# Kernel optimization log

Measured on AMD Instinct MI355X. Metric: run time of the kernel, lower is better.

## Reference

```python
import jax, jax.numpy as jnp
import numpy as np
import math

B, C, F, H, W, K = 2, 4, 512, 8, 1024, 3
DH = F // H

def _rotary(x):
    # lucidrains-style rotary: interleaved pairs, x:[..., seq, d]
    d, seq = x.shape[-1], x.shape[-2]
    inv = 1.0 / (10000.0 ** (jnp.arange(0, d, 2, dtype=jnp.float32) / d))
    freqs = jnp.arange(seq, dtype=jnp.float32)[:, None] * inv[None, :]  # [seq, d/2]
    freqs = jnp.repeat(freqs, 2, axis=-1)                               # [seq, d]
    cos, sin = jnp.cos(freqs), jnp.sin(freqs)
    xp = x.reshape(x.shape[:-1] + (d // 2, 2))
    rot = jnp.stack([-xp[..., 1], xp[..., 0]], axis=-1).reshape(x.shape)
    return x * cos + rot * sin

def _mc_linear(x, w):
    # per-channel position-wise linear: x [b,c,f,w], w [c, f_out, f_in]
    return jnp.einsum('bcfw,cgf->bcgw', x, w)

def _conv(x, w, bias):
    # Conv2d(C, C, (1,K), padding=(0,(K-1)//2)); w [O=c, I=c, 1, K]
    pad = (K - 1) // 2
    y = jax.lax.conv_general_dilated(x, w, (1, 1), [(0, 0), (pad, pad)],
                                     dimension_numbers=('NCHW', 'OIHW', 'NCHW'))
    return y + bias[None, :, None, None]

def _heads(x):
    # [b,c,f,w] -> [b,c,H,w,dh]
    b, c, f, w = x.shape
    return x.transpose(0, 1, 3, 2).reshape(b, c, w, H, DH).transpose(0, 1, 3, 2, 4)

def setup_inputs() -> dict:
    key = jax.random.key(0)
    ks = jax.random.split(key, 12)
    p = lambda k, shp: jax.random.normal(k, shp, dtype=jnp.float32) * 0.02
    return {
        'x': jax.random.normal(ks[0], (B, C, F, W), dtype=jnp.float32),
        'prev_qk': jax.random.normal(ks[1], (B, C, H, W, W), dtype=jnp.float32),
        'mask': jax.random.normal(ks[2], (1, 1, 1, W, W), dtype=jnp.float32),
        'wq_lin': p(ks[3], (C, F, F)), 'wq_conv': p(ks[4], (C, C, 1, K)), 'bq_conv': jnp.zeros((C,), jnp.float32),
        'wk_lin': p(ks[5], (C, F, F)), 'wk_conv': p(ks[6], (C, C, 1, K)), 'bk_conv': jnp.zeros((C,), jnp.float32),
        'wv_lin': p(ks[7], (C, F, F)), 'wv_conv': p(ks[8], (C, C, 1, K)), 'bv_conv': jnp.zeros((C,), jnp.float32),
        'wo_lin': p(ks[9], (C, F, F)),
    }

def reference(x, prev_qk, mask, wq_lin, wq_conv, bq_conv, wk_lin, wk_conv, bk_conv,
              wv_lin, wv_conv, bv_conv, wo_lin):
    b, c, f, w = x.shape
    q = _rotary(_heads(_conv(_mc_linear(x, wq_lin), wq_conv, bq_conv)))   # [b,c,H,w,dh]
    k = _rotary(_heads(_conv(_mc_linear(x, wk_lin), wk_conv, bk_conv)))
    v = _heads(_conv(_mc_linear(x, wv_lin), wv_conv, bv_conv))
    qk = jnp.einsum('bchqd,bchkd->bchqk', q, k) / math.sqrt(f) + prev_qk + mask
    a = jnp.einsum('bchqk,bchkd->bchqd', jax.nn.softmax(qk, axis=-1), v)  # [b,c,H,w,dh]
    a = a.transpose(0, 1, 3, 2, 4).reshape(b, c, w, f).transpose(0, 1, 3, 2)  # [b,c,f,w]
    out = _mc_linear(a, wo_lin)
    return out, qk
```

## Files before the change

### kernel.cpp

```cpp
#include <hip/hip_runtime.h>
#include <hip/hip_bf16.h>
#include <math.h>

typedef unsigned short u16;
typedef unsigned int   u32;
typedef __attribute__((ext_vector_type(8))) short short8;
typedef __attribute__((ext_vector_type(4))) float f32x4;

#define Bn 2
#define Cn 4
#define Fn 512
#define Hn 8
#define Wn 1024
#define DHn 64
#define FW (Fn*Wn)
#define BCFW (Bn*Cn*Fn*Wn)

__device__ __forceinline__ u16 f2bf(float f) {
  u32 u = __builtin_bit_cast(u32, f);
  u += 0x7fffu + ((u >> 16) & 1u);
  return (u16)(u >> 16);
}
__device__ __forceinline__ float bf2f(u16 h) {
  u32 u = ((u32)h) << 16;
  return __builtin_bit_cast(float, u);
}
__device__ __forceinline__ u32 pack2(u16 a, u16 b) { return (u32)a | ((u32)b << 16); }

__global__ __launch_bounds__(256) void wconv_kernel(
    const float* __restrict__ wq, const float* __restrict__ wk,
    const float* __restrict__ wv, const float* __restrict__ wo,
    u16* __restrict__ wb3, u16* __restrict__ wob) {
  int g = blockIdx.x * 256 + threadIdx.x;
  int t = g >> 18;
  int off = (g & 0x3FFFF) * 4;
  const float* src = (t == 0) ? wq : (t == 1) ? wk : (t == 2) ? wv : wo;
  float4 v = *(const float4*)(src + off);
  u16* dst = (t < 3) ? (wb3 + (size_t)t * 1048576 + off) : (wob + off);
  uint2 p;
  p.x = pack2(f2bf(v.x), f2bf(v.y));
  p.y = pack2(f2bf(v.z), f2bf(v.w));
  *(uint2*)dst = p;
}

__global__ __launch_bounds__(256) void xT_kernel(const float* __restrict__ x, u16* __restrict__ xT) {
  __shared__ __align__(16) u16 T[64 * 72];
  int w0 = blockIdx.x * 64, f0 = blockIdx.y * 64, bc = blockIdx.z;
  int tid = threadIdx.x;
  int r = tid >> 2, g = tid & 3;
  const float* src = x + ((size_t)(bc * Fn + f0 + r)) * Wn + w0 + g * 16;
#pragma unroll
  for (int u = 0; u < 4; u++) {
    float4 v = *(const float4*)(src + u * 4);
    int cb = g * 16 + u * 4;
    T[r * 72 + cb + 0] = f2bf(v.x);
    T[r * 72 + cb + 1] = f2bf(v.y);
    T[r * 72 + cb + 2] = f2bf(v.z);
    T[r * 72 + cb + 3] = f2bf(v.w);
  }
  __syncthreads();
  int wl = tid >> 2, fg = tid & 3;
  u16 ov[16];
#pragma unroll
  for (int u = 0; u < 16; u++) ov[u] = T[(fg * 16 + u) * 72 + wl];
  u16* dst = xT + ((size_t)(bc * Wn + w0 + wl)) * Fn + f0 + fg * 16;
  uint4 o0, o1;
  o0.x = pack2(ov[0], ov[1]);  o0.y = pack2(ov[2], ov[3]);
  o0.z = pack2(ov[4], ov[5]);  o0.w = pack2(ov[6], ov[7]);
  o1.x = pack2(ov[8], ov[9]);  o1.y = pack2(ov[10], ov[11]);
  o1.z = pack2(ov[12], ov[13]); o1.w = pack2(ov[14], ov[15]);
  *(uint4*)(dst) = o0;
  *(uint4*)(dst + 8) = o1;
}

__global__ __launch_bounds__(256) void gemm_bt_kernel(
    const u16* __restrict__ Abase, const u16* __restrict__ BTbase,
    u16* __restrict__ Cb, float* __restrict__ Cf) {
  __shared__ __align__(16) u16 As[128 * 40];
  __shared__ __align__(16) u16 Bs[128 * 40];
  int tile = blockIdx.x;
  int bc = blockIdx.y;
  int p = blockIdx.z;
  int m0 = (tile & 3) * 128, n0 = (tile >> 2) * 128;
  const u16* A = Abase + ((size_t)(p * 4 + (bc & 3))) * (512 * 512) + (size_t)m0 * 512;
  const u16* BT = BTbase + (size_t)bc * (1024 * 512) + (size_t)n0 * 512;
  int tid = threadIdx.x, wave = tid >> 6, lane = tid & 63;
  int quad = lane >> 4, l16 = lane & 15;
  int wm = (wave >> 1) * 64, wn = (wave & 1) * 64;
  f32x4 acc[4][4];
#pragma unroll
  for (int i = 0; i < 4; i++)
#pragma unroll
    for (int j = 0; j < 4; j++) acc[i][j] = (f32x4){0.f, 0.f, 0.f, 0.f};
  for (int k0 = 0; k0 < 512; k0 += 32) {
    __syncthreads();
    {
      int c0 = tid, c1 = tid + 256;
      int r = c0 >> 2, o = c0 & 3;
      *(uint4*)&As[r * 40 + o * 8] = *(const uint4*)(A + (size_t)r * 512 + k0 + o * 8);
      *(uint4*)&Bs[r * 40 + o * 8] = *(const uint4*)(BT + (size_t)r * 512 + k0 + o * 8);
      r = c1 >> 2; o = c1 & 3;
      *(uint4*)&As[r * 40 + o * 8] = *(const uint4*)(A + (size_t)r * 512 + k0 + o * 8);
      *(uint4*)&Bs[r * 40 + o * 8] = *(const uint4*)(BT + (size_t)r * 512 + k0 + o * 8);
    }
    __syncthreads();
    short8 af[4], bfr[4];
#pragma unroll
    for (int i = 0; i < 4; i++) af[i] = *(const short8*)&As[(wm + i * 16 + l16) * 40 + quad * 8];
#pragma unroll
    for (int j = 0; j < 4; j++) bfr[j] = *(const short8*)&Bs[(wn + j * 16 + l16) * 40 + quad * 8];
#pragma unroll
    for (int i = 0; i < 4; i++)
#pragma unroll
      for (int j = 0; j < 4; j++)
        acc[i][j] = __builtin_amdgcn_mfma_f32_16x16x32_bf16(af[i], bfr[j], acc[i][j], 0, 0, 0);
  }
  size_t coff = (size_t)(Cb ? (p * 8 + bc) : bc) * FW;
#pragma unroll
  for (int i = 0; i < 4; i++)
#pragma unroll
    for (int j = 0; j < 4; j++)
#pragma unroll
      for (int reg = 0; reg < 4; reg++) {
        int row = m0 + wm + i * 16 + quad * 4 + reg;
        int col = n0 + wn + j * 16 + l16;
        if (Cb) Cb[coff + (size_t)row * 1024 + col] = f2bf(acc[i][j][reg]);
        else    Cf[coff + (size_t)row * 1024 + col] = acc[i][j][reg];
      }
}

__global__ __launch_bounds__(256) void conv_kernel(
    const u16* __restrict__ lin3, u16* __restrict__ conv3,
    const float* __restrict__ wqc, const float* __restrict__ wkc, const float* __restrict__ wvc,
    const float* __restrict__ bq, const float* __restrict__ bk, const float* __restrict__ bv) {
  int w = blockIdx.x * 256 + threadIdx.x;
  int f = blockIdx.y;
  int b = blockIdx.z;
  const float* wcs[3] = {wqc, wkc, wvc};
  const float* bs[3] = {bq, bk, bv};
#pragma unroll
  for (int p = 0; p < 3; p++) {
    const float* wc = wcs[p];
    float acc[4];
#pragma unroll
    for (int o = 0; o < 4; o++) acc[o] = bs[p][o];
#pragma unroll
    for (int i = 0; i < 4; i++) {
      size_t base = ((size_t)((p * 2 + b) * 4 + i) * Fn + f) * Wn + w;
      float xm = (w > 0) ? bf2f(lin3[base - 1]) : 0.f;
      float x0 = bf2f(lin3[base]);
      float xp = (w < Wn - 1) ? bf2f(lin3[base + 1]) : 0.f;
#pragma unroll
      for (int o = 0; o < 4; o++) {
        const float* wr = wc + (o * 4 + i) * 3;
        acc[o] += wr[0] * xm + wr[1] * x0 + wr[2] * xp;
      }
    }
#pragma unroll
    for (int o = 0; o < 4; o++)
      conv3[((size_t)((p * 2 + b) * 4 + o) * Fn + f) * Wn + w] = f2bf(acc[o]);
  }
}

__global__ __launch_bounds__(256) void rot_kernel(
    const u16* __restrict__ conv3, u16* __restrict__ Qb, u16* __restrict__ Kb) {
  __shared__ __align__(16) u16 T[64 * 72];
  int w0 = blockIdx.x * 64;
  int t = blockIdx.y >> 3;
  int h = blockIdx.y & 7;
  int bc = blockIdx.z;
  int b = bc >> 2, c = bc & 3;
  const u16* src = conv3 + ((size_t)((t * 2 + b) * 4 + c) * Fn + h * 64) * Wn;
  int tid = threadIdx.x;
  {
    int dl = tid >> 2, g = tid & 3;
    const u16* s = src + (size_t)dl * Wn + w0 + g * 16;
    *(uint4*)&T[dl * 72 + g * 16] = *(const uint4*)(s);
    *(uint4*)&T[dl * 72 + g * 16 + 8] = *(const uint4*)(s + 8);
  }
  __syncthreads();
  int wl = tid >> 2, dg = tid & 3;
  int pos = w0 + wl;
  u16 ov[16];
#pragma unroll
  for (int u = 0; u < 16; u += 2) {
    int d = dg * 16 + u;
    float x0 = bf2f(T[d * 72 + wl]);
    float x1 = bf2f(T[(d + 1) * 72 + wl]);
    float inv = exp2f(-(float)d * (13.287712379549449f / 64.f));
    float th = (float)pos * inv;
    float sn, cs;
    sincosf(th, &sn, &cs);
    ov[u] = f2bf(x0 * cs - x1 * sn);
    ov[u + 1] = f2bf(x1 * cs + x0 * sn);
  }
  u16* dst = (t == 0 ? Qb : Kb) + ((size_t)(bc * 8 + h) * Wn + pos) * 64 + dg * 16;
  uint4 o0, o1;
  o0.x = pack2(ov[0], ov[1]);  o0.y = pack2(ov[2], ov[3]);
  o0.z = pack2(ov[4], ov[5]);  o0.w = pack2(ov[6], ov[7]);
  o1.x = pack2(ov[8], ov[9]);  o1.y = pack2(ov[10], ov[11]);
  o1.z = pack2(ov[12], ov[13]); o1.w = pack2(ov[14], ov[15]);
  *(uint4*)(dst) = o0;
  *(uint4*)(dst + 8) = o1;
}

__global__ __launch_bounds__(256) void attn_kernel(
    const u16* __restrict__ Qb, const u16* __restrict__ Kb, const u16* __restrict__ Vt,
    const float* __restrict__ prev, const float* __restrict__ maskp,
    float* __restrict__ qkp, u16* __restrict__ Abuf) {
  __shared__ __align__(16) u16 Ks[128 * 72];
  __shared__ __align__(16) u16 Vs[64 * 136];
  __shared__ __align__(16) u16 Ps[128 * 136];
  const int bch = blockIdx.y;
  const int q0 = blockIdx.x * 128;
  const u16* Qg = Qb + (size_t)bch * 65536;
  const u16* Kg = Kb + (size_t)bch * 65536;
  const u16* Vg = Vt + (size_t)bch * 65536;
  const float* prevb = prev + (size_t)bch * 1048576;
  float* qkb = qkp + (size_t)bch * 1048576;
  int tid = threadIdx.x, wave = tid >> 6, lane = tid & 63;
  int quad = lane >> 4, l16 = lane & 15;
  const float SCALE = 0.044194173824159216f;

  short8 qf[2][2];
#pragma unroll
  for (int rt = 0; rt < 2; rt++)
#pragma unroll
    for (int ks = 0; ks < 2; ks++)
      qf[rt][ks] = *(const short8*)(Qg + (size_t)(q0 + wave * 32 + rt * 16 + l16) * 64 + ks * 32 + quad * 8);

  f32x4 oa[2][4];
  float m_run[2][4], l_run[2][4];
#pragma unroll
  for (int rt = 0; rt < 2; rt++)
#pragma unroll
    for (int j = 0; j < 4; j++) {
      oa[rt][j] = (f32x4){0.f, 0.f, 0.f, 0.f};
      m_run[rt][j] = -INFINITY; l_run[rt][j] = 0.f;
    }

  for (int kt = 0; kt < 8; kt++) {
    int k0 = kt * 128;
    __syncthreads();
#pragma unroll
    for (int t = 0; t < 4; t++) {
      int c = tid + 256 * t;
      { int r = c >> 3, of = c & 7;
        *(uint4*)&Ks[r * 72 + of * 8] = *(const uint4*)(Kg + (size_t)(k0 + r) * 64 + of * 8); }
      { int r = c >> 4, of = c & 15;
        *(uint4*)&Vs[r * 136 + of * 8] = *(const uint4*)(Vg + (size_t)r * Wn + k0 + of * 8); }
    }
    __syncthreads();

    f32x4 s[2][8];
#pragma unroll
    for (int rt = 0; rt < 2; rt++)
#pragma unroll
      for (int ct = 0; ct < 8; ct++) s[rt][ct] = (f32x4){0.f, 0.f, 0.f, 0.f};
#pragma unroll
    for (int ct = 0; ct < 8; ct++) {
#pragma unroll
      for (int ks = 0; ks < 2; ks++) {
        short8 kf = *(const short8*)&Ks[(ct * 16 + l16) * 72 + ks * 32 + quad * 8];
        s[0][ct] = __builtin_amdgcn_mfma_f32_16x16x32_bf16(qf[0][ks], kf, s[0][ct], 0, 0, 0);
        s[1][ct] = __builtin_amdgcn_mfma_f32_16x16x32_bf16(qf[1][ks], kf, s[1][ct], 0, 0, 0);
      }
    }
#pragma unroll
    for (int rt = 0; rt < 2; rt++) {
#pragma unroll
      for (int reg = 0; reg < 4; reg++) {
        int rloc = wave * 32 + rt * 16 + quad * 4 + reg;
        int rg = q0 + rloc;
        const float* pr = prevb + (size_t)rg * Wn + k0 + l16;
        const float* mr = maskp + (size_t)rg * Wn + k0 + l16;
        float* qr = qkb + (size_t)rg * Wn + k0 + l16;
        float tv[8];
#pragma unroll
        for (int ct = 0; ct < 8; ct++) {
          tv[ct] = s[rt][ct][reg] * SCALE + pr[ct * 16] + mr[ct * 16];
          qr[ct * 16] = tv[ct];
        }
        float mx = tv[0];
#pragma unroll
        for (int ct = 1; ct < 8; ct++) mx = fmaxf(mx, tv[ct]);
#pragma unroll
        for (int d = 1; d < 16; d <<= 1) mx = fmaxf(mx, __shfl_xor(mx, d));
        float mn = fmaxf(m_run[rt][reg], mx);
        float alpha = __expf(m_run[rt][reg] - mn);
        m_run[rt][reg] = mn;
        float rs = 0.f;
        int prow = rloc * 136;
#pragma unroll
        for (int ct = 0; ct < 8; ct++) {
          float pv = __expf(tv[ct] - mn);
          rs += pv;
          Ps[prow + ct * 16 + l16] = f2bf(pv);
        }
#pragma unroll
        for (int d = 1; d < 16; d <<= 1) rs += __shfl_xor(rs, d);
        l_run[rt][reg] = l_run[rt][reg] * alpha + rs;
#pragma unroll
        for (int jd = 0; jd < 4; jd++) oa[rt][jd][reg] *= alpha;
      }
    }
    __syncthreads();
#pragma unroll
    for (int ks = 0; ks < 4; ks++) {
      short8 pf0 = *(const short8*)&Ps[(wave * 32 + 0 + l16) * 136 + ks * 32 + quad * 8];
      short8 pf1 = *(const short8*)&Ps[(wave * 32 + 16 + l16) * 136 + ks * 32 + quad * 8];
#pragma unroll
      for (int jd = 0; jd < 4; jd++) {
        short8 vf = *(const short8*)&Vs[(jd * 16 + l16) * 136 + ks * 32 + quad * 8];
        oa[0][jd] = __builtin_amdgcn_mfma_f32_16x16x32_bf16(pf0, vf, oa[0][jd], 0, 0, 0);
        oa[1][jd] = __builtin_amdgcn_mfma_f32_16x16x32_bf16(pf1, vf, oa[1][jd], 0, 0, 0);
      }
    }
  }
  int bc = bch >> 3, h = bch & 7;
#pragma unroll
  for (int rt = 0; rt < 2; rt++)
#pragma unroll
    for (int reg = 0; reg < 4; reg++) {
      int rg = q0 + wave * 32 + rt * 16 + quad * 4 + reg;
      float inv_l = 1.f / l_run[rt][reg];
      u16* dst = Abuf + ((size_t)bc * Wn + rg) * Fn + h * 64 + l16;
#pragma unroll
      for (int jd = 0; jd < 4; jd++)
        dst[jd * 16] = f2bf(oa[rt][jd][reg] * inv_l);
    }
}

extern "C" void kernel_launch(void* const* d_in, const int* in_sizes, int n_in,
                              void* d_out, int out_size, void* d_ws, size_t ws_size,
                              hipStream_t stream) {
  (void)in_sizes; (void)n_in; (void)out_size; (void)ws_size;
  const float* x       = (const float*)d_in[0];
  const float* prev    = (const float*)d_in[1];
  const float* mask    = (const float*)d_in[2];
  const float* wq_lin  = (const float*)d_in[3];
  const float* wq_conv = (const float*)d_in[4];
  const float* bq      = (const float*)d_in[5];
  const float* wk_lin  = (const float*)d_in[6];
  const float* wk_conv = (const float*)d_in[7];
  const float* bk      = (const float*)d_in[8];
  const float* wv_lin  = (const float*)d_in[9];
  const float* wv_conv = (const float*)d_in[10];
  const float* bv      = (const float*)d_in[11];
  const float* wo_lin  = (const float*)d_in[12];

  float* outp = (float*)d_out;
  float* qkp  = outp + (size_t)BCFW;

  char* ws = (char*)d_ws;
  u16* xTb   = (u16*)(ws + 0);
  u16* wb3   = (u16*)(ws + ((size_t)8 << 20));
  u16* wob   = (u16*)(ws + ((size_t)14 << 20));
  u16* lin3  = (u16*)(ws + ((size_t)16 << 20));
  u16* conv3 = (u16*)(ws + ((size_t)40 << 20));
  u16* Qbuf  = lin3;
  u16* Kbuf  = lin3 + (size_t)BCFW;
  u16* Abuf  = lin3 + (size_t)2 * BCFW;
  u16* Vt    = conv3 + (size_t)2 * BCFW;

  wconv_kernel<<<4096, 256, 0, stream>>>(wq_lin, wk_lin, wv_lin, wo_lin, wb3, wob);
  xT_kernel<<<dim3(16, 8, 8), 256, 0, stream>>>(x, xTb);
  gemm_bt_kernel<<<dim3(32, 8, 3), 256, 0, stream>>>(wb3, xTb, lin3, nullptr);
  conv_kernel<<<dim3(4, 512, 2), 256, 0, stream>>>(lin3, conv3, wq_conv, wk_conv, wv_conv, bq, bk, bv);
  rot_kernel<<<dim3(16, 16, 8), 256, 0, stream>>>(conv3, Qbuf, Kbuf);
  attn_kernel<<<dim3(8, 64), 256, 0, stream>>>(Qbuf, Kbuf, Vt, prev, mask, qkp, Abuf);
  gemm_bt_kernel<<<dim3(32, 8, 1), 256, 0, stream>>>(wob, Abuf, nullptr, outp);
}
```

Baseline: 828.8 us.

## Split fused attention into parallel QK/stats kernel and PV kernel

```diff
diff --git a/kernel.cpp b/kernel.cpp
--- a/kernel.cpp
+++ b/kernel.cpp
@@ -204,131 +204,157 @@
   *(uint4*)(dst + 8) = o1;
 }
 
-__global__ __launch_bounds__(256) void attn_kernel(
-    const u16* __restrict__ Qb, const u16* __restrict__ Kb, const u16* __restrict__ Vt,
+__global__ __launch_bounds__(256) void qk_kernel(
+    const u16* __restrict__ Qb, const u16* __restrict__ Kb,
     const float* __restrict__ prev, const float* __restrict__ maskp,
-    float* __restrict__ qkp, u16* __restrict__ Abuf) {
+    float* __restrict__ qkp, float2* __restrict__ stats) {
   __shared__ __align__(16) u16 Ks[128 * 72];
-  __shared__ __align__(16) u16 Vs[64 * 136];
-  __shared__ __align__(16) u16 Ps[128 * 136];
-  const int bch = blockIdx.y;
-  const int q0 = blockIdx.x * 128;
+  __shared__ __align__(16) float Sf[64 * 132];
+  const int q0 = blockIdx.x * 64;
+  const int kt = blockIdx.y;
+  const int k0 = kt * 128;
+  const int bch = blockIdx.z;
   const u16* Qg = Qb + (size_t)bch * 65536;
   const u16* Kg = Kb + (size_t)bch * 65536;
-  const u16* Vg = Vt + (size_t)bch * 65536;
   const float* prevb = prev + (size_t)bch * 1048576;
   float* qkb = qkp + (size_t)bch * 1048576;
   int tid = threadIdx.x, wave = tid >> 6, lane = tid & 63;
   int quad = lane >> 4, l16 = lane & 15;
   const float SCALE = 0.044194173824159216f;
 
-  short8 qf[2][2];
-#pragma unroll
-  for (int rt = 0; rt < 2; rt++)
-#pragma unroll
-    for (int ks = 0; ks < 2; ks++)
-      qf[rt][ks] = *(const short8*)(Qg + (size_t)(q0 + wave * 32 + rt * 16 + l16) * 64 + ks * 32 + quad * 8);
-
-  f32x4 oa[2][4];
-  float m_run[2][4], l_run[2][4];
-#pragma unroll
-  for (int rt = 0; rt < 2; rt++)
-#pragma unroll
-    for (int j = 0; j < 4; j++) {
-      oa[rt][j] = (f32x4){0.f, 0.f, 0.f, 0.f};
-      m_run[rt][j] = -INFINITY; l_run[rt][j] = 0.f;
-    }
+  short8 qf[2];
+#pragma unroll
+  for (int ks = 0; ks < 2; ks++)
+    qf[ks] = *(const short8*)(Qg + (size_t)(q0 + wave * 16 + l16) * 64 + ks * 32 + quad * 8);
+
+#pragma unroll
+  for (int t = 0; t < 4; t++) {
+    int c = tid + 256 * t;
+    int r = c >> 3, o = c & 7;
+    *(uint4*)&Ks[r * 72 + o * 8] = *(const uint4*)(Kg + (size_t)(k0 + r) * 64 + o * 8);
+  }
+  __syncthreads();
+
+  f32x4 acc[8];
+#pragma unroll
+  for (int ct = 0; ct < 8; ct++) acc[ct] = (f32x4){0.f, 0.f, 0.f, 0.f};
+#pragma unroll
+  for (int ct = 0; ct < 8; ct++)
+#pragma unroll
+    for (int ks = 0; ks < 2; ks++) {
+      short8 kf = *(const short8*)&Ks[(ct * 16 + l16) * 72 + ks * 32 + quad * 8];
+      acc[ct] = __builtin_amdgcn_mfma_f32_16x16x32_bf16(qf[ks], kf, acc[ct], 0, 0, 0);
+    }
+
+#pragma unroll
+  for (int ct = 0; ct < 8; ct++)
+#pragma unroll
+    for (int reg = 0; reg < 4; reg++)
+      Sf[(wave * 16 + quad * 4 + reg) * 132 + ct * 16 + l16] = acc[ct][reg] * SCALE;
+  __syncthreads();
+
+  int r = tid >> 2, c0 = (tid & 3) * 32;
+  const float* pr = prevb + (size_t)(q0 + r) * Wn + k0 + c0;
+  const float* mr = maskp + (size_t)(q0 + r) * Wn + k0 + c0;
+  float* qr = qkb + (size_t)(q0 + r) * Wn + k0 + c0;
+  float tv[32];
+  float mx = -INFINITY;
+#pragma unroll
+  for (int u = 0; u < 8; u++) {
+    float4 s4 = *(const float4*)&Sf[r * 132 + c0 + u * 4];
+    float4 p4 = *(const float4*)(pr + u * 4);
+    float4 m4 = *(const float4*)(mr + u * 4);
+    float4 t4;
+    t4.x = s4.x + p4.x + m4.x;  t4.y = s4.y + p4.y + m4.y;
+    t4.z = s4.z + p4.z + m4.z;  t4.w = s4.w + p4.w + m4.w;
+    *(float4*)(qr + u * 4) = t4;
+    tv[u * 4 + 0] = t4.x; tv[u * 4 + 1] = t4.y; tv[u * 4 + 2] = t4.z; tv[u * 4 + 3] = t4.w;
+    mx = fmaxf(mx, fmaxf(fmaxf(t4.x, t4.y), fmaxf(t4.z, t4.w)));
+  }
+  mx = fmaxf(mx, __shfl_xor(mx, 1));
+  mx = fmaxf(mx, __shfl_xor(mx, 2));
+  float sum = 0.f;
+#pragma unroll
+  for (int u = 0; u < 32; u++) sum += __expf(tv[u] - mx);
+  sum += __shfl_xor(sum, 1);
+  sum += __shfl_xor(sum, 2);
+  if ((tid & 3) == 0)
+    stats[((size_t)bch * Wn + q0 + r) * 8 + kt] = make_float2(mx, sum);
+}
+
+__global__ __launch_bounds__(256) void pv_kernel(
+    const float* __restrict__ qkp, const u16* __restrict__ Vt,
+    const float2* __restrict__ stats, u16* __restrict__ Abuf) {
+  __shared__ __align__(16) u16 Ps[64 * 136];
+  __shared__ __align__(16) u16 Vs[64 * 136];
+  __shared__ float Mrow[64], Lrow[64];
+  const int q0 = blockIdx.x * 64;
+  const int bch = blockIdx.y;
+  const float* qkb = qkp + (size_t)bch * 1048576;
+  const u16* Vg = Vt + (size_t)bch * 65536;
+  int tid = threadIdx.x, wave = tid >> 6, lane = tid & 63;
+  int quad = lane >> 4, l16 = lane & 15;
+
+  if (tid < 64) {
+    const float2* st = stats + ((size_t)bch * Wn + q0 + tid) * 8;
+    float M = -INFINITY;
+#pragma unroll
+    for (int kt = 0; kt < 8; kt++) M = fmaxf(M, st[kt].x);
+    float L = 0.f;
+#pragma unroll
+    for (int kt = 0; kt < 8; kt++) L += st[kt].y * __expf(st[kt].x - M);
+    Mrow[tid] = M;
+    Lrow[tid] = 1.f / L;
+  }
+
+  f32x4 oa[4];
+#pragma unroll
+  for (int jd = 0; jd < 4; jd++) oa[jd] = (f32x4){0.f, 0.f, 0.f, 0.f};
+
+  int pr_ = tid >> 2, pc_ = (tid & 3) * 32;
+  float Mr, Li;
 
   for (int kt = 0; kt < 8; kt++) {
     int k0 = kt * 128;
     __syncthreads();
+    if (kt == 0) { Mr = Mrow[pr_]; Li = Lrow[pr_]; }
 #pragma unroll
     for (int t = 0; t < 4; t++) {
       int c = tid + 256 * t;
-      { int r = c >> 3, of = c & 7;
-        *(uint4*)&Ks[r * 72 + of * 8] = *(const uint4*)(Kg + (size_t)(k0 + r) * 64 + of * 8); }
-      { int r = c >> 4, of = c & 15;
-        *(uint4*)&Vs[r * 136 + of * 8] = *(const uint4*)(Vg + (size_t)r * Wn + k0 + of * 8); }
+      int r = c >> 4, o = c & 15;
+      *(uint4*)&Vs[r * 136 + o * 8] = *(const uint4*)(Vg + (size_t)r * Wn + k0 + o * 8);
+    }
+    const float* qr = qkb + (size_t)(q0 + pr_) * Wn + k0 + pc_;
+#pragma unroll
+    for (int u = 0; u < 8; u++) {
+      float4 t4 = *(const float4*)(qr + u * 4);
+      u16 p0 = f2bf(__expf(t4.x - Mr) * Li);
+      u16 p1 = f2bf(__expf(t4.y - Mr) * Li);
+      u16 p2 = f2bf(__expf(t4.z - Mr) * Li);
+      u16 p3 = f2bf(__expf(t4.w - Mr) * Li);
+      uint2 pk; pk.x = pack2(p0, p1); pk.y = pack2(p2, p3);
+      *(uint2*)&Ps[pr_ * 136 + pc_ + u * 4] = pk;
     }
     __syncthreads();
-
-    f32x4 s[2][8];
-#pragma unroll
-    for (int rt = 0; rt < 2; rt++)
-#pragma unroll
-      for (int ct = 0; ct < 8; ct++) s[rt][ct] = (f32x4){0.f, 0.f, 0.f, 0.f};
-#pragma unroll
-    for (int ct = 0; ct < 8; ct++) {
-#pragma unroll
-      for (int ks = 0; ks < 2; ks++) {
-        short8 kf = *(const short8*)&Ks[(ct * 16 + l16) * 72 + ks * 32 + quad * 8];
-        s[0][ct] = __builtin_amdgcn_mfma_f32_16x16x32_bf16(qf[0][ks], kf, s[0][ct], 0, 0, 0);
-        s[1][ct] = __builtin_amdgcn_mfma_f32_16x16x32_bf16(qf[1][ks], kf, s[1][ct], 0, 0, 0);
-      }
-    }
-#pragma unroll
-    for (int rt = 0; rt < 2; rt++) {
-#pragma unroll
-      for (int reg = 0; reg < 4; reg++) {
-        int rloc = wave * 32 + rt * 16 + quad * 4 + reg;
-        int rg = q0 + rloc;
-        const float* pr = prevb + (size_t)rg * Wn + k0 + l16;
-        const float* mr = maskp + (size_t)rg * Wn + k0 + l16;
-        float* qr = qkb + (size_t)rg * Wn + k0 + l16;
-        float tv[8];
-#pragma unroll
-        for (int ct = 0; ct < 8; ct++) {
-          tv[ct] = s[rt][ct][reg] * SCALE + pr[ct * 16] + mr[ct * 16];
-          qr[ct * 16] = tv[ct];
-        }
-        float mx = tv[0];
-#pragma unroll
-        for (int ct = 1; ct < 8; ct++) mx = fmaxf(mx, tv[ct]);
-#pragma unroll
-        for (int d = 1; d < 16; d <<= 1) mx = fmaxf(mx, __shfl_xor(mx, d));
-        float mn = fmaxf(m_run[rt][reg], mx);
-        float alpha = __expf(m_run[rt][reg] - mn);
-        m_run[rt][reg] = mn;
-        float rs = 0.f;
-        int prow = rloc * 136;
-#pragma unroll
-        for (int ct = 0; ct < 8; ct++) {
-          float pv = __expf(tv[ct] - mn);
-          rs += pv;
-          Ps[prow + ct * 16 + l16] = f2bf(pv);
-        }
-#pragma unroll
-        for (int d = 1; d < 16; d <<= 1) rs += __shfl_xor(rs, d);
-        l_run[rt][reg] = l_run[rt][reg] * alpha + rs;
-#pragma unroll
-        for (int jd = 0; jd < 4; jd++) oa[rt][jd][reg] *= alpha;
-      }
-    }
-    __syncthreads();
 #pragma unroll
     for (int ks = 0; ks < 4; ks++) {
-      short8 pf0 = *(const short8*)&Ps[(wave * 32 + 0 + l16) * 136 + ks * 32 + quad * 8];
-      short8 pf1 = *(const short8*)&Ps[(wave * 32 + 16 + l16) * 136 + ks * 32 + quad * 8];
+      short8 pf = *(const short8*)&Ps[(wave * 16 + l16) * 136 + ks * 32 + quad * 8];
 #pragma unroll
       for (int jd = 0; jd < 4; jd++) {
         short8 vf = *(const short8*)&Vs[(jd * 16 + l16) * 136 + ks * 32 + quad * 8];
-        oa[0][jd] = __builtin_amdgcn_mfma_f32_16x16x32_bf16(pf0, vf, oa[0][jd], 0, 0, 0);
-        oa[1][jd] = __builtin_amdgcn_mfma_f32_16x16x32_bf16(pf1, vf, oa[1][jd], 0, 0, 0);
+        oa[jd] = __builtin_amdgcn_mfma_f32_16x16x32_bf16(pf, vf, oa[jd], 0, 0, 0);
       }
     }
   }
   int bc = bch >> 3, h = bch & 7;
 #pragma unroll
-  for (int rt = 0; rt < 2; rt++)
-#pragma unroll
-    for (int reg = 0; reg < 4; reg++) {
-      int rg = q0 + wave * 32 + rt * 16 + quad * 4 + reg;
-      float inv_l = 1.f / l_run[rt][reg];
-      u16* dst = Abuf + ((size_t)bc * Wn + rg) * Fn + h * 64 + l16;
-#pragma unroll
-      for (int jd = 0; jd < 4; jd++)
-        dst[jd * 16] = f2bf(oa[rt][jd][reg] * inv_l);
-    }
+  for (int reg = 0; reg < 4; reg++) {
+    int rg = q0 + wave * 16 + quad * 4 + reg;
+    u16* dst = Abuf + ((size_t)bc * Wn + rg) * Fn + h * 64 + l16;
+#pragma unroll
+    for (int jd = 0; jd < 4; jd++)
+      dst[jd * 16] = f2bf(oa[jd][reg]);
+  }
 }
 
 extern "C" void kernel_launch(void* const* d_in, const int* in_sizes, int n_in,
@@ -362,12 +388,14 @@
   u16* Kbuf  = lin3 + (size_t)BCFW;
   u16* Abuf  = lin3 + (size_t)2 * BCFW;
   u16* Vt    = conv3 + (size_t)2 * BCFW;
+  float2* stats = (float2*)(ws + ((size_t)40 << 20));
 
   wconv_kernel<<<4096, 256, 0, stream>>>(wq_lin, wk_lin, wv_lin, wo_lin, wb3, wob);
   xT_kernel<<<dim3(16, 8, 8), 256, 0, stream>>>(x, xTb);
   gemm_bt_kernel<<<dim3(32, 8, 3), 256, 0, stream>>>(wb3, xTb, lin3, nullptr);
   conv_kernel<<<dim3(4, 512, 2), 256, 0, stream>>>(lin3, conv3, wq_conv, wk_conv, wv_conv, bq, bk, bv);
   rot_kernel<<<dim3(16, 16, 8), 256, 0, stream>>>(conv3, Qbuf, Kbuf);
-  attn_kernel<<<dim3(8, 64), 256, 0, stream>>>(Qbuf, Kbuf, Vt, prev, mask, qkp, Abuf);
+  qk_kernel<<<dim3(16, 8, 64), 256, 0, stream>>>(Qbuf, Kbuf, prev, mask, qkp, stats);
+  pv_kernel<<<dim3(16, 64), 256, 0, stream>>>(qkp, Vt, stats, Abuf);
   gemm_bt_kernel<<<dim3(32, 8, 1), 256, 0, stream>>>(wob, Abuf, nullptr, outp);
 }
```

Measured after the change: 688.0 us. 17.0% less time.
